# Kernel optimization log

Measured on AMD Instinct MI355X. Metric: run time of the kernel, lower is better.

## Reference

```python
import jax, jax.numpy as jnp
import numpy as np

N_NODES = 50000
N_EDGES = 800000
IN_C = 64
HID = 128
OUT_C = 2
N_GRAPHS = 64


def setup_inputs() -> dict:
    key = jax.random.key(0)
    ks = jax.random.split(key, 12)
    x = jax.random.normal(ks[0], (N_NODES, IN_C), dtype=jnp.float32)
    edge_index = jax.random.randint(ks[1], (2, N_EDGES), 0, N_NODES, dtype=jnp.int64)
    batch = jnp.sort(jax.random.randint(ks[2], (N_NODES,), 0, N_GRAPHS, dtype=jnp.int64))
    def glorot(k, shape):
        lim = float(np.sqrt(6.0 / (shape[0] + shape[1])))
        return jax.random.uniform(k, shape, dtype=jnp.float32, minval=-lim, maxval=lim)
    return {
        "x": x,
        "edge_index": edge_index,
        "batch": batch,
        "W1": glorot(ks[3], (IN_C, HID)),  "b1": jnp.zeros((HID,), jnp.float32),
        "W2": glorot(ks[4], (HID, HID)),   "b2": jnp.zeros((HID,), jnp.float32),
        "Wm1": glorot(ks[5], (HID, HID)),  "bm1": jnp.zeros((HID,), jnp.float32),
        "Wm2": glorot(ks[6], (HID, OUT_C)), "bm2": jnp.zeros((OUT_C,), jnp.float32),
    }


def reference(x, edge_index, batch, W1, b1, W2, b2, Wm1, bm1, Wm2, bm2):
    N = x.shape[0]
    # GCN normalization with self-loops (PyG GCNConv defaults)
    loops = jnp.arange(N, dtype=edge_index.dtype)
    src = jnp.concatenate([edge_index[0], loops])  # message sources
    dst = jnp.concatenate([edge_index[1], loops])  # aggregation targets
    deg = jax.ops.segment_sum(jnp.ones(dst.shape, x.dtype), dst, num_segments=N)
    dinv = jnp.where(deg > 0, jax.lax.rsqrt(deg), 0.0)
    norm = dinv[src] * dinv[dst]  # [E+N]

    def gcn_conv(h, W, b):
        h = h @ W                         # transform first (PyG order)
        msg = h[src] * norm[:, None]      # gather + normalize
        return jax.ops.segment_sum(msg, dst, num_segments=N) + b  # scatter-add

    h = jax.nn.relu(gcn_conv(x, W1, b1))
    # dropout is identity in eval mode
    h = gcn_conv(h, W2, b2)

    # global mean pool over graphs
    sums = jax.ops.segment_sum(h, batch, num_segments=N_GRAPHS)
    cnt = jax.ops.segment_sum(jnp.ones((N,), h.dtype), batch, num_segments=N_GRAPHS)
    g = sums / jnp.maximum(cnt, 1.0)[:, None]  # [G, HID]

    g = jax.nn.relu(g @ Wm1 + bm1)
    return g @ Wm2 + bm2  # [G, OUT_C]
```

## Files before the change

### kernel.cpp

```cpp
#include <hip/hip_runtime.h>
#include <stdint.h>

#define N_NODES 50000
#define N_EDGES 800000
#define IN_C 64
#define HID 128
#define OUT_C 2
#define N_GRAPHS 64
#define NBUCK 196
#define BCAP 6144
#define ECH 4096

typedef long long i64;
typedef __attribute__((ext_vector_type(8))) short bf8;
typedef __attribute__((ext_vector_type(4))) float f32x4;

__device__ __forceinline__ float bf2f(ushort h) {
    return __uint_as_float(((uint)h) << 16);
}
__device__ __forceinline__ ushort f2bf(float f) {
    uint x = __float_as_uint(f);
    uint r = x + 0x7fffu + ((x >> 16) & 1u);
    return (ushort)(r >> 16);
}
__device__ __forceinline__ float loadf(const void* p, size_t i, int bf) {
    return bf ? bf2f(((const ushort*)p)[i]) : ((const float*)p)[i];
}
__device__ __forceinline__ int clampi(int v, int lo, int hi) {
    return min(max(v, lo), hi);
}

__device__ __forceinline__ int edge_src(const void* ei, int e, int wide) {
    return wide ? (int)((const i64*)ei)[e] : ((const int*)ei)[e];
}
__device__ __forceinline__ int edge_dst(const void* ei, int e, int wide) {
    return wide ? (int)((const i64*)ei)[N_EDGES + e] : ((const int*)ei)[N_EDGES + e];
}
__device__ __forceinline__ i64 batch_at(const void* b, int i, int wide) {
    return wide ? ((const i64*)b)[i] : (i64)((const int*)b)[i];
}

__global__ __launch_bounds__(256) void k_init(const uint* __restrict__ braw,
                                              const uint* __restrict__ xraw,
                                              int* __restrict__ bcnt,
                                              float* __restrict__ gbuf,
                                              int* __restrict__ iflag,
                                              int* __restrict__ fflag) {
    int i = blockIdx.x * blockDim.x + threadIdx.x;
    if (i < N_GRAPHS * HID) gbuf[i] = 0.f;
    if (i < NBUCK) bcnt[i] = 0;
    if (blockIdx.x == 0) {
        __shared__ uint si[128];
        __shared__ int sf[256];
        int t = threadIdx.x;
        if (t < 128) si[t] = (t < 100) ? braw[25001 + 2 * t] : 0u;
        uint e = (xraw[t] >> 7) & 0xFFu;
        sf[t] = (e >= 100u && e <= 140u) ? 1 : 0;
        __syncthreads();
        for (int off = 128; off > 0; off >>= 1) {
            if (t < off) {
                sf[t] += sf[t + off];
                if (off <= 64 && t < 64) si[t] |= si[t + off];
            }
            __syncthreads();
        }
        if (t == 0) {
            *iflag = (si[0] == 0u) ? 1 : 0;
            *fflag = (sf[0] >= 192) ? 1 : 0;
        }
    }
}

__global__ __launch_bounds__(1024) void k_binA(const void* __restrict__ ei,
                                               const int* __restrict__ iflag,
                                               const int* __restrict__ fflag,
                                               const void* __restrict__ W1,
                                               const void* __restrict__ W2,
                                               ushort* __restrict__ Wt1,
                                               ushort* __restrict__ Wt2,
                                               int* __restrict__ bcnt,
                                               uint2* __restrict__ bmem) {
    int t = threadIdx.x;
    if (t < 256 && blockIdx.x < (IN_C * HID + HID * HID) / 256) {
        int ff = *fflag;
        int idx = blockIdx.x * 256 + t;
        if (idx < IN_C * HID) {
            int k = idx >> 7, n = idx & 127;
            Wt1[n * IN_C + k] = f2bf(loadf(W1, idx, ff));
        } else {
            int j = idx - IN_C * HID;
            int k = j >> 7, n = j & 127;
            Wt2[n * HID + k] = f2bf(loadf(W2, j, ff));
        }
    }
    int wide = *iflag;
    __shared__ int cnt[NBUCK];
    __shared__ int obase[NBUCK];
    __shared__ int run[NBUCK];
    __shared__ int gbase[NBUCK];
    __shared__ int sc[256];
    __shared__ uint2 stage[ECH];
    int e0 = blockIdx.x * ECH;
    int m = min(ECH, N_EDGES - e0);
    for (int i = t; i < NBUCK; i += 1024) cnt[i] = 0;
    __syncthreads();
    for (int i = t; i < m; i += 1024) {
        int d = edge_dst(ei, e0 + i, wide);
        atomicAdd(&cnt[d >> 8], 1);
    }
    __syncthreads();
    int cv = (t < NBUCK) ? cnt[t] : 0;
    if (t < 256) sc[t] = cv;
    __syncthreads();
    for (int off = 1; off < 256; off <<= 1) {
        int v = (t >= off && t < 256) ? sc[t - off] : 0;
        __syncthreads();
        if (t < 256) sc[t] += v;
        __syncthreads();
    }
    if (t < NBUCK) {
        int ex = sc[t] - cv;
        obase[t] = ex;
        run[t] = ex;
        gbase[t] = (cv > 0) ? atomicAdd(&bcnt[t], cv) : 0;
    }
    __syncthreads();
    for (int i = t; i < m; i += 1024) {
        int s = edge_src(ei, e0 + i, wide);
        int d = edge_dst(ei, e0 + i, wide);
        int slot = atomicAdd(&run[d >> 8], 1);
        uint2 pr;
        pr.x = (uint)s;
        pr.y = (uint)d;
        stage[slot] = pr;
    }
    __syncthreads();
    for (int i = t; i < m; i += 1024) {
        uint2 pr = stage[i];
        int b = (int)(pr.y >> 8);
        int pos = gbase[b] + (i - obase[b]);
        if (pos < BCAP) bmem[(size_t)b * BCAP + pos] = pr;
    }
}

__global__ __launch_bounds__(1024) void k_binB(const uint2* __restrict__ bmem,
                                               const int* __restrict__ bcnt,
                                               const void* __restrict__ x,
                                               const int* __restrict__ fflag,
                                               int* __restrict__ offs,
                                               int* __restrict__ csr,
                                               float* __restrict__ dinv,
                                               ushort* __restrict__ Y1) {
    int b = blockIdx.x;
    int t = threadIdx.x;
    int node0 = b << 8;
    __shared__ int sc[256];
    __shared__ int degl[256];
    __shared__ int run[256];
    __shared__ float sdinv[256];
    __shared__ int sbase, scnt;
    __shared__ int stage[BCAP];
    int v = (t < NBUCK) ? bcnt[t] : 0;
    if (t < 256) sc[t] = v;
    __syncthreads();
    for (int off = 1; off < 256; off <<= 1) {
        int u = (t >= off && t < 256) ? sc[t - off] : 0;
        __syncthreads();
        if (t < 256) sc[t] += u;
        __syncthreads();
    }
    if (t == b) {
        int c = clampi(v, 0, BCAP);
        scnt = c;
        sbase = clampi(sc[t] - v, 0, N_EDGES - c);
    }
    if (t < 256) degl[t] = 0;
    __syncthreads();
    int cnt = scnt;
    int base = sbase;
    for (int i = t; i < cnt; i += 1024) {
        uint2 pr = bmem[(size_t)b * BCAP + i];
        atomicAdd(&degl[pr.y & 255], 1);
    }
    __syncthreads();
    int dv = (t < 256) ? degl[t] : 0;
    if (t < 256) sc[t] = dv;
    __syncthreads();
    for (int off = 1; off < 256; off <<= 1) {
        int u = (t >= off && t < 256) ? sc[t - off] : 0;
        __syncthreads();
        if (t < 256) sc[t] += u;
        __syncthreads();
    }
    if (t < 256) {
        int ex = sc[t] - dv;
        run[t] = ex;
        float di = rsqrtf((float)(dv + 1));
        sdinv[t] = di;
        int n = node0 + t;
        if (n < N_NODES) {
            offs[n] = base + ex;
            dinv[n] = di;
        }
    }
    if (b == 0 && t == 0) offs[N_NODES] = N_EDGES;
    __syncthreads();
    for (int i = t; i < cnt; i += 1024) {
        uint2 pr = bmem[(size_t)b * BCAP + i];
        int slot = atomicAdd(&run[pr.y & 255], 1);
        stage[clampi(slot, 0, BCAP - 1)] = (int)pr.x;
    }
    __syncthreads();
    for (int i = t; i < cnt; i += 1024) csr[base + i] = stage[i];
    int ff = *fflag;
    for (int idx = t; idx < 256 * (IN_C / 4); idx += 1024) {
        int nl = idx >> 4, c4 = (idx & 15) * 4;
        int nn = node0 + nl;
        if (nn < N_NODES) {
            float x0, x1, x2, x3;
            if (ff) {
                const ushort* xp = (const ushort*)x + (size_t)nn * IN_C + c4;
                ushort4 u = *(const ushort4*)xp;
                x0 = bf2f(u.x); x1 = bf2f(u.y); x2 = bf2f(u.z); x3 = bf2f(u.w);
            } else {
                const float* xp = (const float*)x + (size_t)nn * IN_C + c4;
                float4 vv = *(const float4*)xp;
                x0 = vv.x; x1 = vv.y; x2 = vv.z; x3 = vv.w;
            }
            float di = sdinv[nl];
            ushort4 o;
            o.x = f2bf(x0 * di); o.y = f2bf(x1 * di);
            o.z = f2bf(x2 * di); o.w = f2bf(x3 * di);
            *(ushort4*)(Y1 + (size_t)nn * IN_C + c4) = o;
        }
    }
}

__global__ __launch_bounds__(256) void k_aggM(const ushort* __restrict__ Y1,
                                              const float* __restrict__ dinv,
                                              const int* __restrict__ offs,
                                              const int* __restrict__ csr,
                                              ushort* __restrict__ M) {
    int n = (blockIdx.x * blockDim.x + threadIdx.x) >> 4;
    int lane = threadIdx.x & 15;
    if (n >= N_NODES) return;
    const uint* y32 = (const uint*)Y1;
    size_t rb = (size_t)n * 32;
    uint s0 = y32[rb + lane];
    uint s1 = y32[rb + lane + 16];
    float a0 = bf2f((ushort)(s0 & 0xffffu));
    float a1 = bf2f((ushort)(s0 >> 16));
    float a2 = bf2f((ushort)(s1 & 0xffffu));
    float a3 = bf2f((ushort)(s1 >> 16));
    int s = offs[n];
    int e = min(offs[n + 1], s + 4096);
    int i = s;
    for (; i + 8 <= e; i += 8) {
        uint u0[8], u1[8];
#pragma unroll
        for (int k = 0; k < 8; k++) {
            size_t r = (size_t)csr[i + k] * 32;
            u0[k] = y32[r + lane];
            u1[k] = y32[r + lane + 16];
        }
#pragma unroll
        for (int k = 0; k < 8; k++) {
            a0 += bf2f((ushort)(u0[k] & 0xffffu));
            a1 += bf2f((ushort)(u0[k] >> 16));
            a2 += bf2f((ushort)(u1[k] & 0xffffu));
            a3 += bf2f((ushort)(u1[k] >> 16));
        }
    }
    for (; i < e; i++) {
        size_t r = (size_t)csr[i] * 32;
        uint u0 = y32[r + lane];
        uint u1 = y32[r + lane + 16];
        a0 += bf2f((ushort)(u0 & 0xffffu));
        a1 += bf2f((ushort)(u0 >> 16));
        a2 += bf2f((ushort)(u1 & 0xffffu));
        a3 += bf2f((ushort)(u1 >> 16));
    }
    float dv = dinv[n];
    ((uint*)M)[rb + lane] = ((uint)f2bf(a1 * dv) << 16) | (uint)f2bf(a0 * dv);
    ((uint*)M)[rb + lane + 16] = ((uint)f2bf(a3 * dv) << 16) | (uint)f2bf(a2 * dv);
}

__global__ __launch_bounds__(256) void k_agg128(const ushort* __restrict__ hs,
                                                const float* __restrict__ dinv,
                                                const int* __restrict__ offs,
                                                const int* __restrict__ csr,
                                                ushort* __restrict__ out) {
    int n = (blockIdx.x * blockDim.x + threadIdx.x) >> 5;
    int lane = threadIdx.x & 31;
    if (n >= N_NODES) return;
    const uint* hs32 = (const uint*)hs;
    size_t rb = (size_t)n * 64;
    uint s0 = hs32[rb + lane];
    uint s1 = hs32[rb + lane + 32];
    float a0 = bf2f((ushort)(s0 & 0xffffu));
    float a1 = bf2f((ushort)(s0 >> 16));
    float a2 = bf2f((ushort)(s1 & 0xffffu));
    float a3 = bf2f((ushort)(s1 >> 16));
    int s = offs[n];
    int e = min(offs[n + 1], s + 4096);
    int i = s;
    for (; i + 8 <= e; i += 8) {
        uint u0[8], u1[8];
#pragma unroll
        for (int k = 0; k < 8; k++) {
            size_t r = (size_t)csr[i + k] * 64;
            u0[k] = hs32[r + lane];
            u1[k] = hs32[r + lane + 32];
        }
#pragma unroll
        for (int k = 0; k < 8; k++) {
            a0 += bf2f((ushort)(u0[k] & 0xffffu));
            a1 += bf2f((ushort)(u0[k] >> 16));
            a2 += bf2f((ushort)(u1[k] & 0xffffu));
            a3 += bf2f((ushort)(u1[k] >> 16));
        }
    }
    for (; i < e; i++) {
        size_t r = (size_t)csr[i] * 64;
        uint u0 = hs32[r + lane];
        uint u1 = hs32[r + lane + 32];
        a0 += bf2f((ushort)(u0 & 0xffffu));
        a1 += bf2f((ushort)(u0 >> 16));
        a2 += bf2f((ushort)(u1 & 0xffffu));
        a3 += bf2f((ushort)(u1 >> 16));
    }
    float dv = dinv[n];
    ((uint*)out)[rb + lane] = ((uint)f2bf(a1 * dv) << 16) | (uint)f2bf(a0 * dv);
    ((uint*)out)[rb + lane + 32] = ((uint)f2bf(a3 * dv) << 16) | (uint)f2bf(a2 * dv);
}

template <int K>
__global__ __launch_bounds__(256) void k_gemm_f(const ushort* __restrict__ A,
                                                const ushort* __restrict__ Wt,
                                                const int* __restrict__ fflag,
                                                const float* __restrict__ dinv,
                                                const void* __restrict__ bias,
                                                ushort* __restrict__ out) {
    int ff = *fflag;
    int wave = threadIdx.x >> 6;
    int lane = threadIdx.x & 63;
    int m16 = lane & 15;
    int q = lane >> 4;
    int rowbase = blockIdx.x * 64 + wave * 16;
    int arow = min(rowbase + m16, N_NODES - 1);

    f32x4 acc[8];
#pragma unroll
    for (int t = 0; t < 8; t++) acc[t] = (f32x4){0.f, 0.f, 0.f, 0.f};

#pragma unroll
    for (int kc = 0; kc < K; kc += 32) {
        bf8 a = *(const bf8*)(A + (size_t)arow * K + kc + q * 8);
#pragma unroll
        for (int t = 0; t < 8; t++) {
            bf8 b = *(const bf8*)(Wt + (size_t)(t * 16 + m16) * K + kc + q * 8);
            acc[t] = __builtin_amdgcn_mfma_f32_16x16x32_bf16(a, b, acc[t], 0, 0, 0);
        }
    }

    float dv[4];
    int rowok[4];
#pragma unroll
    for (int r = 0; r < 4; r++) {
        int row = rowbase + q * 4 + r;
        rowok[r] = (row < N_NODES);
        dv[r] = rowok[r] ? dinv[row] : 1.f;
    }
#pragma unroll
    for (int t = 0; t < 8; t++) {
        int col = t * 16 + m16;
        float bv = loadf(bias, col, ff);
#pragma unroll
        for (int r = 0; r < 4; r++) {
            int row = rowbase + q * 4 + r;
            if (rowok[r]) {
                float v = fmaxf(acc[t][r] + bv, 0.f) * dv[r];
                out[(size_t)row * HID + col] = f2bf(v);
            }
        }
    }
}

__global__ __launch_bounds__(256) void k_gemm_pool(const ushort* __restrict__ A,
                                                   const ushort* __restrict__ Wt,
                                                   const void* __restrict__ batch,
                                                   const int* __restrict__ iflag,
                                                   float* __restrict__ gsum) {
    const int K = HID;
    int wide = *iflag;
    int tid = threadIdx.x;
    int wave = tid >> 6;
    int lane = tid & 63;
    int m16 = lane & 15;
    int q = lane >> 4;
    int rowbase = blockIdx.x * 64 + wave * 16;
    int arow = min(rowbase + m16, N_NODES - 1);

    __shared__ float sacc[64][HID];
    __shared__ int sbg[64];

    if (tid < 64) {
        int n = blockIdx.x * 64 + tid;
        int g = (n < N_NODES) ? (int)batch_at(batch, n, wide) : -1;
        sbg[tid] = (g < 0 || g >= N_GRAPHS) ? -1 : g;
    }

    f32x4 acc[8];
#pragma unroll
    for (int t = 0; t < 8; t++) acc[t] = (f32x4){0.f, 0.f, 0.f, 0.f};

#pragma unroll
    for (int kc = 0; kc < K; kc += 32) {
        bf8 a = *(const bf8*)(A + (size_t)arow * K + kc + q * 8);
#pragma unroll
        for (int t = 0; t < 8; t++) {
            bf8 b = *(const bf8*)(Wt + (size_t)(t * 16 + m16) * K + kc + q * 8);
            acc[t] = __builtin_amdgcn_mfma_f32_16x16x32_bf16(a, b, acc[t], 0, 0, 0);
        }
    }

#pragma unroll
    for (int t = 0; t < 8; t++) {
        int col = t * 16 + m16;
#pragma unroll
        for (int r = 0; r < 4; r++) {
            int rl = wave * 16 + q * 4 + r;
            int row = rowbase + q * 4 + r;
            sacc[rl][col] = (row < N_NODES) ? acc[t][r] : 0.f;
        }
    }
    __syncthreads();

    int col = tid & 127;
    int half = tid >> 7;
    int gcur = -1;
    float a = 0.f;
    for (int r = half * 32; r < half * 32 + 32; r++) {
        int g = sbg[r];
        if (g != gcur) {
            if (gcur >= 0) atomicAdd(&gsum[gcur * HID + col], a);
            a = 0.f;
            gcur = g;
        }
        a += sacc[r][col];
    }
    if (gcur >= 0) atomicAdd(&gsum[gcur * HID + col], a);
}

__global__ void k_mlp(const float* __restrict__ gsum, const void* __restrict__ batch,
                      const int* __restrict__ iflag, const void* __restrict__ b2,
                      const void* __restrict__ Wm1, const void* __restrict__ bm1,
                      const void* __restrict__ Wm2, const void* __restrict__ bm2,
                      const int* __restrict__ fflag, float* __restrict__ out) {
    int ff = *fflag;
    int wide = *iflag;
    int gr = blockIdx.x;
    int c = threadIdx.x;
    int lo = 0, hi = N_NODES;
    while (lo < hi) { int m = (lo + hi) >> 1; if (batch_at(batch, m, wide) < (i64)gr) lo = m + 1; else hi = m; }
    int s = lo;
    lo = s; hi = N_NODES;
    while (lo < hi) { int m = (lo + hi) >> 1; if (batch_at(batch, m, wide) < (i64)(gr + 1)) lo = m + 1; else hi = m; }
    float cnt = (float)(lo - s);

    __shared__ float sg[HID];
    __shared__ float r0[HID], r1[HID];
    sg[c] = gsum[gr * HID + c] / fmaxf(cnt, 1.0f) + loadf(b2, c, ff);
    __syncthreads();
    float acc = loadf(bm1, c, ff);
#pragma unroll 8
    for (int k = 0; k < HID; k++) acc += sg[k] * loadf(Wm1, k * HID + c, ff);
    float hid = fmaxf(acc, 0.f);
    r0[c] = hid * loadf(Wm2, c * OUT_C + 0, ff);
    r1[c] = hid * loadf(Wm2, c * OUT_C + 1, ff);
    __syncthreads();
    for (int off = 64; off > 0; off >>= 1) {
        if (c < off) { r0[c] += r0[c + off]; r1[c] += r1[c + off]; }
        __syncthreads();
    }
    if (c == 0) {
        out[gr * OUT_C + 0] = r0[0] + loadf(bm2, 0, ff);
        out[gr * OUT_C + 1] = r1[0] + loadf(bm2, 1, ff);
    }
}


extern "C" void kernel_launch(void* const* d_in, const int* in_sizes, int n_in,
                              void* d_out, int out_size, void* d_ws, size_t ws_size,
                              hipStream_t stream) {
    const void* x     = d_in[0];
    const void* ei    = d_in[1];
    const void* batch = d_in[2];
    const void* W1  = d_in[3];
    const void* b1  = d_in[4];
    const void* W2  = d_in[5];
    const void* b2  = d_in[6];
    const void* Wm1 = d_in[7];
    const void* bm1 = d_in[8];
    const void* Wm2 = d_in[9];
    const void* bm2 = d_in[10];

    char* p = (char*)d_ws;
    auto alloc = [&](size_t bytes) {
        char* r = p;
        p += (bytes + 255) & ~(size_t)255;
        return r;
    };
    int*    iflag  = (int*)alloc(4);
    int*    fflag  = (int*)alloc(4);
    int*    bcnt   = (int*)alloc(NBUCK * 4);
    uint2*  bmem   = (uint2*)alloc((size_t)NBUCK * BCAP * 8);
    float*  dinv   = (float*)alloc(N_NODES * 4);
    int*    offs   = (int*)alloc((N_NODES + 1) * 4);
    int*    csr    = (int*)alloc(N_EDGES * 4);
    ushort* Wt1    = (ushort*)alloc(IN_C * HID * 2);
    ushort* Wt2    = (ushort*)alloc(HID * HID * 2);
    ushort* Y1     = (ushort*)alloc((size_t)N_NODES * IN_C * 2);
    ushort* Mbuf   = (ushort*)alloc((size_t)N_NODES * IN_C * 2);
    ushort* h1s    = (ushort*)alloc((size_t)N_NODES * HID * 2);
    ushort* N2     = (ushort*)alloc((size_t)N_NODES * HID * 2);
    float*  gbuf   = (float*)alloc(N_GRAPHS * HID * 4);

    k_init<<<(N_GRAPHS * HID + 255) / 256, 256, 0, stream>>>(
        (const uint*)batch, (const uint*)x, bcnt, gbuf, iflag, fflag);
    k_binA<<<(N_EDGES + ECH - 1) / ECH, 1024, 0, stream>>>(
        ei, iflag, fflag, W1, W2, Wt1, Wt2, bcnt, bmem);
    k_binB<<<NBUCK, 1024, 0, stream>>>(bmem, bcnt, x, fflag, offs, csr, dinv, Y1);

    k_aggM<<<(N_NODES * 16 + 255) / 256, 256, 0, stream>>>(Y1, dinv, offs, csr, Mbuf);
    k_gemm_f<IN_C><<<(N_NODES + 63) / 64, 256, 0, stream>>>(Mbuf, Wt1, fflag, dinv, b1, h1s);
    k_agg128<<<(N_NODES * 32 + 255) / 256, 256, 0, stream>>>(h1s, dinv, offs, csr, N2);
    k_gemm_pool<<<(N_NODES + 63) / 64, 256, 0, stream>>>(N2, Wt2, batch, iflag, gbuf);

    k_mlp<<<N_GRAPHS, HID, 0, stream>>>(gbuf, batch, iflag, b2, Wm1, bm1, Wm2, bm2, fflag, (float*)d_out);
}
```

Baseline: 204.2 us.

## Fuse all GCN stages into one cooperative persistent kernel with grid syncs

```diff
diff --git a/kernel.cpp b/kernel.cpp
--- a/kernel.cpp
+++ b/kernel.cpp
@@ -1,5 +1,8 @@
 #include <hip/hip_runtime.h>
+#include <hip/hip_cooperative_groups.h>
 #include <stdint.h>
+
+namespace cg = cooperative_groups;
 
 #define N_NODES 50000
 #define N_EDGES 800000
@@ -10,6 +13,9 @@
 #define NBUCK 196
 #define BCAP 6144
 #define ECH 4096
+#define MECH 3125
+#define MCHUNK 256
+#define NTILE 782
 
 typedef long long i64;
 typedef __attribute__((ext_vector_type(8))) short bf8;
@@ -39,6 +45,457 @@
 __device__ __forceinline__ i64 batch_at(const void* b, int i, int wide) {
     return wide ? ((const i64*)b)[i] : (i64)((const int*)b)[i];
 }
+
+
+struct SmA {
+    int cnt[NBUCK]; int obase[NBUCK]; int run[NBUCK]; int gbase[NBUCK];
+    int sc[256]; uint2 stage[MECH];
+};
+struct SmB {
+    int sc[256]; int degl[256]; int run[256]; float sdinv[256];
+    int sbase, scnt; int stage[BCAP];
+};
+struct SmP {
+    float sacc[64][HID]; int sbg[64];
+};
+struct SmM {
+    float sg[8][HID]; float r0[8][HID]; float r1[8][HID];
+};
+struct SmI {
+    uint si[128]; int sf[256];
+};
+union MegaSm { SmA a; SmB b; SmP p; SmM m; SmI i; };
+
+__global__ __launch_bounds__(1024) void k_mega(
+    const void* __restrict__ x, const void* __restrict__ ei,
+    const void* __restrict__ batch,
+    const void* __restrict__ W1, const void* __restrict__ b1,
+    const void* __restrict__ W2, const void* __restrict__ b2,
+    const void* __restrict__ Wm1, const void* __restrict__ bm1,
+    const void* __restrict__ Wm2, const void* __restrict__ bm2,
+    int* __restrict__ bcnt, uint2* __restrict__ bmem,
+    float* __restrict__ dinv, int* __restrict__ offs, int* __restrict__ csr,
+    ushort* __restrict__ Wt1, ushort* __restrict__ Wt2,
+    ushort* __restrict__ Y1, ushort* __restrict__ Mbuf,
+    ushort* __restrict__ h1s, ushort* __restrict__ N2,
+    float* __restrict__ gbuf, int* __restrict__ iflag, int* __restrict__ fflag,
+    float* __restrict__ outp) {
+    cg::grid_group grid = cg::this_grid();
+    __shared__ MegaSm sm;
+    int tid = threadIdx.x;
+    int gsz = gridDim.x;
+
+    {
+        int g = blockIdx.x * 1024 + tid;
+        if (g < NBUCK) bcnt[g] = 0;
+        if (g < N_GRAPHS * HID) gbuf[g] = 0.f;
+        if (blockIdx.x == 0 && tid < 256) {
+            const uint* braw = (const uint*)batch;
+            const uint* xraw = (const uint*)x;
+            if (tid < 128) sm.i.si[tid] = (tid < 100) ? braw[25001 + 2 * tid] : 0u;
+            uint e = (xraw[tid] >> 7) & 0xFFu;
+            sm.i.sf[tid] = (e >= 100u && e <= 140u) ? 1 : 0;
+        }
+        __syncthreads();
+        if (blockIdx.x == 0 && tid < 128) {
+            for (int off = 128; off > 0; off >>= 1) {
+                if (tid < off && tid + off < 256) sm.i.sf[tid] += sm.i.sf[tid + off];
+                if (tid < off && off <= 64) sm.i.si[tid] |= sm.i.si[tid + off];
+                __syncthreads();
+            }
+            if (tid == 0) {
+                *iflag = (sm.i.si[0] == 0u) ? 1 : 0;
+                *fflag = (sm.i.sf[0] >= 192) ? 1 : 0;
+            }
+        }
+    }
+    __threadfence();
+    grid.sync();
+
+    {
+        int ff = *fflag;
+        for (int w = blockIdx.x; w < 24; w += gsz) {
+            int idx = w * 1024 + tid;
+            if (idx < IN_C * HID) {
+                int k = idx >> 7, n = idx & 127;
+                Wt1[n * IN_C + k] = f2bf(loadf(W1, idx, ff));
+            } else if (idx < IN_C * HID + HID * HID) {
+                int j = idx - IN_C * HID;
+                int k = j >> 7, n = j & 127;
+                Wt2[n * HID + k] = f2bf(loadf(W2, j, ff));
+            }
+        }
+        int wide = *iflag;
+        for (int ch = blockIdx.x; ch < MCHUNK; ch += gsz) {
+            int e0 = ch * MECH;
+            __syncthreads();
+            for (int i = tid; i < NBUCK; i += 1024) sm.a.cnt[i] = 0;
+            __syncthreads();
+            for (int i = tid; i < MECH; i += 1024) {
+                int d = edge_dst(ei, e0 + i, wide);
+                atomicAdd(&sm.a.cnt[d >> 8], 1);
+            }
+            __syncthreads();
+            int cv = (tid < NBUCK) ? sm.a.cnt[tid] : 0;
+            if (tid < 256) sm.a.sc[tid] = cv;
+            __syncthreads();
+            for (int off = 1; off < 256; off <<= 1) {
+                int v = (tid >= off && tid < 256) ? sm.a.sc[tid - off] : 0;
+                __syncthreads();
+                if (tid < 256) sm.a.sc[tid] += v;
+                __syncthreads();
+            }
+            if (tid < NBUCK) {
+                int ex = sm.a.sc[tid] - cv;
+                sm.a.obase[tid] = ex;
+                sm.a.run[tid] = ex;
+                sm.a.gbase[tid] = (cv > 0) ? atomicAdd(&bcnt[tid], cv) : 0;
+            }
+            __syncthreads();
+            for (int i = tid; i < MECH; i += 1024) {
+                int s = edge_src(ei, e0 + i, wide);
+                int d = edge_dst(ei, e0 + i, wide);
+                int slot = atomicAdd(&sm.a.run[d >> 8], 1);
+                uint2 pr; pr.x = (uint)s; pr.y = (uint)d;
+                sm.a.stage[slot] = pr;
+            }
+            __syncthreads();
+            for (int i = tid; i < MECH; i += 1024) {
+                uint2 pr = sm.a.stage[i];
+                int b = (int)(pr.y >> 8);
+                int pos = sm.a.gbase[b] + (i - sm.a.obase[b]);
+                if (pos < BCAP) bmem[(size_t)b * BCAP + pos] = pr;
+            }
+        }
+    }
+    __threadfence();
+    grid.sync();
+
+    {
+        int ff = *fflag;
+        for (int bk = blockIdx.x; bk < NBUCK; bk += gsz) {
+            int node0 = bk << 8;
+            __syncthreads();
+            int v = (tid < NBUCK) ? bcnt[tid] : 0;
+            if (tid < 256) sm.b.sc[tid] = v;
+            __syncthreads();
+            for (int off = 1; off < 256; off <<= 1) {
+                int u = (tid >= off && tid < 256) ? sm.b.sc[tid - off] : 0;
+                __syncthreads();
+                if (tid < 256) sm.b.sc[tid] += u;
+                __syncthreads();
+            }
+            if (tid == bk) {
+                int c = clampi(v, 0, BCAP);
+                sm.b.scnt = c;
+                sm.b.sbase = clampi(sm.b.sc[tid] - v, 0, N_EDGES - c);
+            }
+            if (tid < 256) sm.b.degl[tid] = 0;
+            __syncthreads();
+            int cnt = sm.b.scnt;
+            int base = sm.b.sbase;
+            for (int i = tid; i < cnt; i += 1024) {
+                uint2 pr = bmem[(size_t)bk * BCAP + i];
+                atomicAdd(&sm.b.degl[pr.y & 255], 1);
+            }
+            __syncthreads();
+            int dv = (tid < 256) ? sm.b.degl[tid] : 0;
+            if (tid < 256) sm.b.sc[tid] = dv;
+            __syncthreads();
+            for (int off = 1; off < 256; off <<= 1) {
+                int u = (tid >= off && tid < 256) ? sm.b.sc[tid - off] : 0;
+                __syncthreads();
+                if (tid < 256) sm.b.sc[tid] += u;
+                __syncthreads();
+            }
+            if (tid < 256) {
+                int ex = sm.b.sc[tid] - dv;
+                sm.b.run[tid] = ex;
+                float di = rsqrtf((float)(dv + 1));
+                sm.b.sdinv[tid] = di;
+                int n = node0 + tid;
+                if (n < N_NODES) { offs[n] = base + ex; dinv[n] = di; }
+            }
+            if (bk == 0 && tid == 0) offs[N_NODES] = N_EDGES;
+            __syncthreads();
+            for (int i = tid; i < cnt; i += 1024) {
+                uint2 pr = bmem[(size_t)bk * BCAP + i];
+                int slot = atomicAdd(&sm.b.run[pr.y & 255], 1);
+                sm.b.stage[clampi(slot, 0, BCAP - 1)] = (int)pr.x;
+            }
+            __syncthreads();
+            for (int i = tid; i < cnt; i += 1024) csr[base + i] = sm.b.stage[i];
+            for (int idx = tid; idx < 256 * (IN_C / 4); idx += 1024) {
+                int nl = idx >> 4, c4 = (idx & 15) * 4;
+                int nn = node0 + nl;
+                if (nn < N_NODES) {
+                    float x0, x1, x2, x3;
+                    if (ff) {
+                        ushort4 u = *(const ushort4*)((const ushort*)x + (size_t)nn * IN_C + c4);
+                        x0 = bf2f(u.x); x1 = bf2f(u.y); x2 = bf2f(u.z); x3 = bf2f(u.w);
+                    } else {
+                        float4 vv = *(const float4*)((const float*)x + (size_t)nn * IN_C + c4);
+                        x0 = vv.x; x1 = vv.y; x2 = vv.z; x3 = vv.w;
+                    }
+                    float di = sm.b.sdinv[nl];
+                    ushort4 o;
+                    o.x = f2bf(x0 * di); o.y = f2bf(x1 * di);
+                    o.z = f2bf(x2 * di); o.w = f2bf(x3 * di);
+                    *(ushort4*)(Y1 + (size_t)nn * IN_C + c4) = o;
+                }
+            }
+        }
+    }
+    __threadfence();
+    grid.sync();
+
+    {
+        int g = blockIdx.x * 1024 + tid;
+        int lane = g & 15;
+        int step = (gsz * 1024) >> 4;
+        const uint* y32 = (const uint*)Y1;
+        for (int n = g >> 4; n < N_NODES; n += step) {
+            size_t rb = (size_t)n * 32;
+            uint s0 = y32[rb + lane];
+            uint s1 = y32[rb + lane + 16];
+            float a0 = bf2f((ushort)(s0 & 0xffffu));
+            float a1 = bf2f((ushort)(s0 >> 16));
+            float a2 = bf2f((ushort)(s1 & 0xffffu));
+            float a3 = bf2f((ushort)(s1 >> 16));
+            int s = offs[n];
+            int e = min(offs[n + 1], s + 4096);
+            int i = s;
+            for (; i + 8 <= e; i += 8) {
+                uint u0[8], u1[8];
+#pragma unroll
+                for (int k = 0; k < 8; k++) {
+                    size_t r = (size_t)csr[i + k] * 32;
+                    u0[k] = y32[r + lane];
+                    u1[k] = y32[r + lane + 16];
+                }
+#pragma unroll
+                for (int k = 0; k < 8; k++) {
+                    a0 += bf2f((ushort)(u0[k] & 0xffffu));
+                    a1 += bf2f((ushort)(u0[k] >> 16));
+                    a2 += bf2f((ushort)(u1[k] & 0xffffu));
+                    a3 += bf2f((ushort)(u1[k] >> 16));
+                }
+            }
+            for (; i < e; i++) {
+                size_t r = (size_t)csr[i] * 32;
+                uint u0 = y32[r + lane];
+                uint u1 = y32[r + lane + 16];
+                a0 += bf2f((ushort)(u0 & 0xffffu));
+                a1 += bf2f((ushort)(u0 >> 16));
+                a2 += bf2f((ushort)(u1 & 0xffffu));
+                a3 += bf2f((ushort)(u1 >> 16));
+            }
+            float dvv = dinv[n];
+            ((uint*)Mbuf)[rb + lane] = ((uint)f2bf(a1 * dvv) << 16) | (uint)f2bf(a0 * dvv);
+            ((uint*)Mbuf)[rb + lane + 16] = ((uint)f2bf(a3 * dvv) << 16) | (uint)f2bf(a2 * dvv);
+        }
+    }
+    __threadfence();
+    grid.sync();
+
+    {
+        int ff = *fflag;
+        int group = tid >> 8;
+        int local = tid & 255;
+        int subwave = local >> 6;
+        int lane = tid & 63;
+        int m16 = lane & 15, q = lane >> 4;
+        for (int tb = blockIdx.x * 4 + group; tb < NTILE; tb += gsz * 4) {
+            int rowbase = tb * 64 + subwave * 16;
+            int arow = min(rowbase + m16, N_NODES - 1);
+            f32x4 acc[8];
+#pragma unroll
+            for (int t = 0; t < 8; t++) acc[t] = (f32x4){0.f, 0.f, 0.f, 0.f};
+#pragma unroll
+            for (int kc = 0; kc < IN_C; kc += 32) {
+                bf8 a = *(const bf8*)(Mbuf + (size_t)arow * IN_C + kc + q * 8);
+#pragma unroll
+                for (int t = 0; t < 8; t++) {
+                    bf8 b = *(const bf8*)(Wt1 + (size_t)(t * 16 + m16) * IN_C + kc + q * 8);
+                    acc[t] = __builtin_amdgcn_mfma_f32_16x16x32_bf16(a, b, acc[t], 0, 0, 0);
+                }
+            }
+            float dvr[4];
+            int rowok[4];
+#pragma unroll
+            for (int r = 0; r < 4; r++) {
+                int row = rowbase + q * 4 + r;
+                rowok[r] = (row < N_NODES);
+                dvr[r] = rowok[r] ? dinv[row] : 1.f;
+            }
+#pragma unroll
+            for (int t = 0; t < 8; t++) {
+                int col = t * 16 + m16;
+                float bv = loadf(b1, col, ff);
+#pragma unroll
+                for (int r = 0; r < 4; r++) {
+                    int row = rowbase + q * 4 + r;
+                    if (rowok[r]) {
+                        float v = fmaxf(acc[t][r] + bv, 0.f) * dvr[r];
+                        h1s[(size_t)row * HID + col] = f2bf(v);
+                    }
+                }
+            }
+        }
+    }
+    __threadfence();
+    grid.sync();
+
+    {
+        int g = blockIdx.x * 1024 + tid;
+        int lane = g & 31;
+        int step = (gsz * 1024) >> 5;
+        const uint* hs32 = (const uint*)h1s;
+        for (int n = g >> 5; n < N_NODES; n += step) {
+            size_t rb = (size_t)n * 64;
+            uint s0 = hs32[rb + lane];
+            uint s1 = hs32[rb + lane + 32];
+            float a0 = bf2f((ushort)(s0 & 0xffffu));
+            float a1 = bf2f((ushort)(s0 >> 16));
+            float a2 = bf2f((ushort)(s1 & 0xffffu));
+            float a3 = bf2f((ushort)(s1 >> 16));
+            int s = offs[n];
+            int e = min(offs[n + 1], s + 4096);
+            int i = s;
+            for (; i + 8 <= e; i += 8) {
+                uint u0[8], u1[8];
+#pragma unroll
+                for (int k = 0; k < 8; k++) {
+                    size_t r = (size_t)csr[i + k] * 64;
+                    u0[k] = hs32[r + lane];
+                    u1[k] = hs32[r + lane + 32];
+                }
+#pragma unroll
+                for (int k = 0; k < 8; k++) {
+                    a0 += bf2f((ushort)(u0[k] & 0xffffu));
+                    a1 += bf2f((ushort)(u0[k] >> 16));
+                    a2 += bf2f((ushort)(u1[k] & 0xffffu));
+                    a3 += bf2f((ushort)(u1[k] >> 16));
+                }
+            }
+            for (; i < e; i++) {
+                size_t r = (size_t)csr[i] * 64;
+                uint u0 = hs32[r + lane];
+                uint u1 = hs32[r + lane + 32];
+                a0 += bf2f((ushort)(u0 & 0xffffu));
+                a1 += bf2f((ushort)(u0 >> 16));
+                a2 += bf2f((ushort)(u1 & 0xffffu));
+                a3 += bf2f((ushort)(u1 >> 16));
+            }
+            float dvv = dinv[n];
+            ((uint*)N2)[rb + lane] = ((uint)f2bf(a1 * dvv) << 16) | (uint)f2bf(a0 * dvv);
+            ((uint*)N2)[rb + lane + 32] = ((uint)f2bf(a3 * dvv) << 16) | (uint)f2bf(a2 * dvv);
+        }
+    }
+    __threadfence();
+    grid.sync();
+
+    {
+        int wide = *iflag;
+        int wave = tid >> 6;
+        int strip = wave & 3;
+        int ksl = wave >> 2;
+        int lane = tid & 63;
+        int m16 = lane & 15, q = lane >> 4;
+        for (int tile = blockIdx.x; tile < NTILE; tile += gsz) {
+            for (int i = tid; i < 64 * HID; i += 1024) ((float*)sm.p.sacc)[i] = 0.f;
+            if (tid < 64) {
+                int n = tile * 64 + tid;
+                int g = (n < N_NODES) ? (int)batch_at(batch, n, wide) : -1;
+                sm.p.sbg[tid] = (g < 0 || g >= N_GRAPHS) ? -1 : g;
+            }
+            __syncthreads();
+            int rowbase = tile * 64 + strip * 16;
+            int arow = min(rowbase + m16, N_NODES - 1);
+            int kc = ksl * 32;
+            f32x4 acc[8];
+#pragma unroll
+            for (int t = 0; t < 8; t++) acc[t] = (f32x4){0.f, 0.f, 0.f, 0.f};
+            bf8 a = *(const bf8*)(N2 + (size_t)arow * HID + kc + q * 8);
+#pragma unroll
+            for (int t = 0; t < 8; t++) {
+                bf8 b = *(const bf8*)(Wt2 + (size_t)(t * 16 + m16) * HID + kc + q * 8);
+                acc[t] = __builtin_amdgcn_mfma_f32_16x16x32_bf16(a, b, acc[t], 0, 0, 0);
+            }
+#pragma unroll
+            for (int t = 0; t < 8; t++) {
+                int col = t * 16 + m16;
+#pragma unroll
+                for (int r = 0; r < 4; r++) {
+                    int rl = strip * 16 + q * 4 + r;
+                    int row = rowbase + q * 4 + r;
+                    if (row < N_NODES) atomicAdd(&sm.p.sacc[rl][col], acc[t][r]);
+                }
+            }
+            __syncthreads();
+            int col = tid & 127;
+            int rc = tid >> 7;
+            int gcur = -1;
+            float aa = 0.f;
+            for (int r = rc * 8; r < rc * 8 + 8; r++) {
+                int g = sm.p.sbg[r];
+                if (g != gcur) {
+                    if (gcur >= 0) atomicAdd(&gbuf[gcur * HID + col], aa);
+                    aa = 0.f;
+                    gcur = g;
+                }
+                aa += sm.p.sacc[r][col];
+            }
+            if (gcur >= 0) atomicAdd(&gbuf[gcur * HID + col], aa);
+            __syncthreads();
+        }
+    }
+    __threadfence();
+    grid.sync();
+
+    {
+        int ff = *fflag;
+        int wide = *iflag;
+        int group = tid >> 7;
+        int c = tid & 127;
+        int gr = blockIdx.x * 8 + group;
+        bool act = (gr < N_GRAPHS);
+        if (blockIdx.x * 8 < N_GRAPHS) {
+            float cntf = 1.f;
+            if (act) {
+                int lo = 0, hi = N_NODES;
+                while (lo < hi) { int m = (lo + hi) >> 1; if (batch_at(batch, m, wide) < (i64)gr) lo = m + 1; else hi = m; }
+                int s = lo;
+                lo = s; hi = N_NODES;
+                while (lo < hi) { int m = (lo + hi) >> 1; if (batch_at(batch, m, wide) < (i64)(gr + 1)) lo = m + 1; else hi = m; }
+                cntf = fmaxf((float)(lo - s), 1.0f);
+                sm.m.sg[group][c] = gbuf[gr * HID + c] / cntf + loadf(b2, c, ff);
+            }
+            __syncthreads();
+            if (act) {
+                float acc = loadf(bm1, c, ff);
+#pragma unroll 8
+                for (int k = 0; k < HID; k++) acc += sm.m.sg[group][k] * loadf(Wm1, k * HID + c, ff);
+                float hid = fmaxf(acc, 0.f);
+                sm.m.r0[group][c] = hid * loadf(Wm2, c * OUT_C + 0, ff);
+                sm.m.r1[group][c] = hid * loadf(Wm2, c * OUT_C + 1, ff);
+            }
+            __syncthreads();
+            for (int off = 64; off > 0; off >>= 1) {
+                if (act && c < off) {
+                    sm.m.r0[group][c] += sm.m.r0[group][c + off];
+                    sm.m.r1[group][c] += sm.m.r1[group][c + off];
+                }
+                __syncthreads();
+            }
+            if (act && c == 0) {
+                outp[gr * OUT_C + 0] = sm.m.r0[group][0] + loadf(bm2, 0, ff);
+                outp[gr * OUT_C + 1] = sm.m.r1[group][0] + loadf(bm2, 1, ff);
+            }
+        }
+    }
+}
+
 
 __global__ __launch_bounds__(256) void k_init(const uint* __restrict__ braw,
                                               const uint* __restrict__ xraw,
@@ -129,9 +586,7 @@
         int s = edge_src(ei, e0 + i, wide);
         int d = edge_dst(ei, e0 + i, wide);
         int slot = atomicAdd(&run[d >> 8], 1);
-        uint2 pr;
-        pr.x = (uint)s;
-        pr.y = (uint)d;
+        uint2 pr; pr.x = (uint)s; pr.y = (uint)d;
         stage[slot] = pr;
     }
     __syncthreads();
@@ -198,10 +653,7 @@
         float di = rsqrtf((float)(dv + 1));
         sdinv[t] = di;
         int n = node0 + t;
-        if (n < N_NODES) {
-            offs[n] = base + ex;
-            dinv[n] = di;
-        }
+        if (n < N_NODES) { offs[n] = base + ex; dinv[n] = di; }
     }
     if (b == 0 && t == 0) offs[N_NODES] = N_EDGES;
     __syncthreads();
@@ -219,12 +671,10 @@
         if (nn < N_NODES) {
             float x0, x1, x2, x3;
             if (ff) {
-                const ushort* xp = (const ushort*)x + (size_t)nn * IN_C + c4;
-                ushort4 u = *(const ushort4*)xp;
+                ushort4 u = *(const ushort4*)((const ushort*)x + (size_t)nn * IN_C + c4);
                 x0 = bf2f(u.x); x1 = bf2f(u.y); x2 = bf2f(u.z); x3 = bf2f(u.w);
             } else {
-                const float* xp = (const float*)x + (size_t)nn * IN_C + c4;
-                float4 vv = *(const float4*)xp;
+                float4 vv = *(const float4*)((const float*)x + (size_t)nn * IN_C + c4);
                 x0 = vv.x; x1 = vv.y; x2 = vv.z; x3 = vv.w;
             }
             float di = sdinv[nl];
@@ -352,7 +802,6 @@
     f32x4 acc[8];
 #pragma unroll
     for (int t = 0; t < 8; t++) acc[t] = (f32x4){0.f, 0.f, 0.f, 0.f};
-
 #pragma unroll
     for (int kc = 0; kc < K; kc += 32) {
         bf8 a = *(const bf8*)(A + (size_t)arow * K + kc + q * 8);
@@ -362,7 +811,6 @@
             acc[t] = __builtin_amdgcn_mfma_f32_16x16x32_bf16(a, b, acc[t], 0, 0, 0);
         }
     }
-
     float dv[4];
     int rowok[4];
 #pragma unroll
@@ -409,11 +857,9 @@
         int g = (n < N_NODES) ? (int)batch_at(batch, n, wide) : -1;
         sbg[tid] = (g < 0 || g >= N_GRAPHS) ? -1 : g;
     }
-
     f32x4 acc[8];
 #pragma unroll
     for (int t = 0; t < 8; t++) acc[t] = (f32x4){0.f, 0.f, 0.f, 0.f};
-
 #pragma unroll
     for (int kc = 0; kc < K; kc += 32) {
         bf8 a = *(const bf8*)(A + (size_t)arow * K + kc + q * 8);
@@ -423,7 +869,6 @@
             acc[t] = __builtin_amdgcn_mfma_f32_16x16x32_bf16(a, b, acc[t], 0, 0, 0);
         }
     }
-
 #pragma unroll
     for (int t = 0; t < 8; t++) {
         int col = t * 16 + m16;
@@ -435,7 +880,6 @@
         }
     }
     __syncthreads();
-
     int col = tid & 127;
     int half = tid >> 7;
     int gcur = -1;
@@ -525,17 +969,42 @@
     ushort* h1s    = (ushort*)alloc((size_t)N_NODES * HID * 2);
     ushort* N2     = (ushort*)alloc((size_t)N_NODES * HID * 2);
     float*  gbuf   = (float*)alloc(N_GRAPHS * HID * 4);
-
-    k_init<<<(N_GRAPHS * HID + 255) / 256, 256, 0, stream>>>(
-        (const uint*)batch, (const uint*)x, bcnt, gbuf, iflag, fflag);
-    k_binA<<<(N_EDGES + ECH - 1) / ECH, 1024, 0, stream>>>(
-        ei, iflag, fflag, W1, W2, Wt1, Wt2, bcnt, bmem);
-    k_binB<<<NBUCK, 1024, 0, stream>>>(bmem, bcnt, x, fflag, offs, csr, dinv, Y1);
-
-    k_aggM<<<(N_NODES * 16 + 255) / 256, 256, 0, stream>>>(Y1, dinv, offs, csr, Mbuf);
-    k_gemm_f<IN_C><<<(N_NODES + 63) / 64, 256, 0, stream>>>(Mbuf, Wt1, fflag, dinv, b1, h1s);
-    k_agg128<<<(N_NODES * 32 + 255) / 256, 256, 0, stream>>>(h1s, dinv, offs, csr, N2);
-    k_gemm_pool<<<(N_NODES + 63) / 64, 256, 0, stream>>>(N2, Wt2, batch, iflag, gbuf);
-
-    k_mlp<<<N_GRAPHS, HID, 0, stream>>>(gbuf, batch, iflag, b2, Wm1, bm1, Wm2, bm2, fflag, (float*)d_out);
-}
+    float*  outp   = (float*)d_out;
+
+    bool ok = false;
+    int dev = 0, coop = 0, ncu = 0, maxB = 0;
+    if (hipGetDevice(&dev) == hipSuccess &&
+        hipDeviceGetAttribute(&coop, hipDeviceAttributeCooperativeLaunch, dev) == hipSuccess &&
+        coop &&
+        hipDeviceGetAttribute(&ncu, hipDeviceAttributeMultiprocessorCount, dev) == hipSuccess &&
+        hipOccupancyMaxActiveBlocksPerMultiprocessor(&maxB, (const void*)k_mega, 1024, 0) == hipSuccess &&
+        maxB >= 1) {
+        int grid = ncu * maxB;
+        if (grid > 1024) grid = 1024;
+        void* args[] = {
+            (void*)&x, (void*)&ei, (void*)&batch,
+            (void*)&W1, (void*)&b1, (void*)&W2, (void*)&b2,
+            (void*)&Wm1, (void*)&bm1, (void*)&Wm2, (void*)&bm2,
+            (void*)&bcnt, (void*)&bmem, (void*)&dinv, (void*)&offs, (void*)&csr,
+            (void*)&Wt1, (void*)&Wt2, (void*)&Y1, (void*)&Mbuf,
+            (void*)&h1s, (void*)&N2, (void*)&gbuf,
+            (void*)&iflag, (void*)&fflag, (void*)&outp};
+        hipError_t e = hipLaunchCooperativeKernel((const void*)k_mega, dim3(grid),
+                                                  dim3(1024), args, 0, stream);
+        if (e == hipSuccess) ok = true;
+        else (void)hipGetLastError();
+    }
+
+    if (!ok) {
+        k_init<<<(N_GRAPHS * HID + 255) / 256, 256, 0, stream>>>(
+            (const uint*)batch, (const uint*)x, bcnt, gbuf, iflag, fflag);
+        k_binA<<<(N_EDGES + ECH - 1) / ECH, 1024, 0, stream>>>(
+            ei, iflag, fflag, W1, W2, Wt1, Wt2, bcnt, bmem);
+        k_binB<<<NBUCK, 1024, 0, stream>>>(bmem, bcnt, x, fflag, offs, csr, dinv, Y1);
+        k_aggM<<<(N_NODES * 16 + 255) / 256, 256, 0, stream>>>(Y1, dinv, offs, csr, Mbuf);
+        k_gemm_f<IN_C><<<(N_NODES + 63) / 64, 256, 0, stream>>>(Mbuf, Wt1, fflag, dinv, b1, h1s);
+        k_agg128<<<(N_NODES * 32 + 255) / 256, 256, 0, stream>>>(h1s, dinv, offs, csr, N2);
+        k_gemm_pool<<<(N_NODES + 63) / 64, 256, 0, stream>>>(N2, Wt2, batch, iflag, gbuf);
+        k_mlp<<<N_GRAPHS, HID, 0, stream>>>(gbuf, batch, iflag, b2, Wm1, bm1, Wm2, bm2, fflag, outp);
+    }
+}
```

Result: no change. 203.5 us (-0.4%).
